# Kernel optimization log

Measured on AMD Instinct MI355X. Metric: run time of the kernel, lower is better.

The kernel has to match this reference:

```python
import jax, jax.numpy as jnp
import numpy as np

NUM_AUTHORS = 100000
NUM_PAPERS = 150000
EMB_DIM = 64
N_EDGES = 3200000
BATCH = 65536
EPS = 1e-8


def setup_inputs() -> dict:
    key = jax.random.key(0)
    k = jax.random.split(key, 6)
    return {
        "author_emb": jax.random.normal(k[0], (NUM_AUTHORS, EMB_DIM), dtype=jnp.float32) * 0.01,
        "paper_emb": jax.random.normal(k[1], (NUM_PAPERS, EMB_DIM), dtype=jnp.float32) * 0.01,
        "authors": jax.random.randint(k[2], (BATCH,), 0, NUM_AUTHORS),
        "papers": jax.random.randint(k[3], (BATCH,), 0, NUM_PAPERS),
        "edge_author": jax.random.randint(k[4], (N_EDGES,), 0, NUM_AUTHORS),
        "edge_paper": jax.random.randint(k[5], (N_EDGES,), 0, NUM_PAPERS),
    }


def _write_conv(a_emb, p_emb, edge_author, edge_paper, norm, u_sw, i_sw):
    """GCN-style bipartite conv with symmetric degree normalization and
    degree-gated self term (u_sw/i_sw ~= 1 only for isolated nodes)."""
    # messages author -> paper over 'like' edges
    msg_ap = a_emb[edge_author] * norm[:, None]            # [E, D]
    new_p = i_sw * p_emb + jax.ops.segment_sum(msg_ap, edge_paper, num_segments=NUM_PAPERS)
    # messages paper -> author over 'rev_like' edges
    msg_pa = p_emb[edge_paper] * norm[:, None]             # [E, D]
    new_a = u_sw * a_emb + jax.ops.segment_sum(msg_pa, edge_author, num_segments=NUM_AUTHORS)
    return new_a, new_p


def reference(author_emb, paper_emb, authors, papers, edge_author, edge_paper):
    ones_e = jnp.ones((N_EDGES,), dtype=jnp.float32)
    author_deg = jax.ops.segment_sum(ones_e, edge_author, num_segments=NUM_AUTHORS)  # out-deg 'like'
    paper_deg = jax.ops.segment_sum(ones_e, edge_paper, num_segments=NUM_PAPERS)     # out-deg 'rev_like'
    u_sw = (1.0 - author_deg / (author_deg + EPS))[:, None]   # [Na, 1]
    i_sw = (1.0 - paper_deg / (paper_deg + EPS))[:, None]     # [Np, 1]
    # symmetric normalization per edge: 1/sqrt(deg_a * deg_p)
    norm = jax.lax.rsqrt((author_deg[edge_author] + EPS) * (paper_deg[edge_paper] + EPS))  # [E]

    a1, p1 = _write_conv(author_emb, paper_emb, edge_author, edge_paper, norm, u_sw, i_sw)
    a2, p2 = _write_conv(a1, p1, edge_author, edge_paper, norm, u_sw, i_sw)

    final_author = author_emb + a1 + a2   # l_author = [0,1,2]
    final_paper = paper_emb + p1 + p2     # l_paper = [0,1,2]

    latest_author = final_author[authors]  # [B, D]
    latest_paper = final_paper[papers]     # [B, D]
    predict = jax.nn.sigmoid(jnp.sum(latest_author * latest_paper, axis=1))  # [B]
    return predict, latest_author, latest_paper
```

## Files before the change

kernel.cpp:

```cpp
#include <hip/hip_runtime.h>
#include <hip/hip_bf16.h>
#include <math.h>

#define NA 100000
#define NP 150000
#define EMB 64
#define NE 3200000
#define BATCH 65536
#define EPS 1e-8f
#define F8 128.0f
#define INVF8 (1.0f / 128.0f)

#define SH_A 8
#define SH_P 9
#define NB_A ((NA + (1 << SH_A) - 1) >> SH_A)
#define NB_P ((NP + (1 << SH_P) - 1) >> SH_P)
#define NBT (NB_A + NB_P)
#define CAP_A 9216
#define CAP_P 12288
#define TOT_A (NB_A * CAP_A)
#define TOT_P (NB_P * CAP_P)
#define PACK_SH 18
#define PACK_MASK ((1u << PACK_SH) - 1)
#define CHUNK 8192
#define NOENT 0xFFFFFFFFu

typedef float f32x2 __attribute__((ext_vector_type(2)));

#if defined(__has_builtin)
#if __has_builtin(__builtin_amdgcn_cvt_pk_f32_fp8) && __has_builtin(__builtin_amdgcn_cvt_pk_fp8_f32)
#define HW_FP8 1
#endif
#endif

__device__ inline unsigned pk_fp8x4(float a, float b, float c, float d) {
#ifdef HW_FP8
    int t = __builtin_amdgcn_cvt_pk_fp8_f32(a, b, 0, false);
    t = __builtin_amdgcn_cvt_pk_fp8_f32(c, d, t, true);
    return (unsigned)t;
#else
    auto enc = [](float x) -> unsigned {
        union { float f; unsigned u; } t; t.f = x;
        unsigned s = t.u >> 31; int e = (int)((t.u >> 23) & 0xFF) - 127;
        unsigned m = (t.u >> 20) & 7;
        int E = e + 7;
        if (E <= 0) return s << 7;
        if (E > 15) { E = 15; m = 7; }
        return (s << 7) | ((unsigned)E << 3) | m;
    };
    return enc(a) | (enc(b) << 8) | (enc(c) << 16) | (enc(d) << 24);
#endif
}

__device__ inline f32x2 up_fp8x2(unsigned v, bool hi) {
#ifdef HW_FP8
    return hi ? __builtin_amdgcn_cvt_pk_f32_fp8((int)v, true)
              : __builtin_amdgcn_cvt_pk_f32_fp8((int)v, false);
#else
    auto dec = [](unsigned b) -> float {
        unsigned s = b >> 7, e = (b >> 3) & 0xF, m = b & 7;
        if (e == 0) return (s ? -1.0f : 1.0f) * (float)m * 0.001953125f;
        union { unsigned u; float f; } t;
        t.u = (s << 31) | ((e + 120) << 23) | (m << 20);
        return t.f;
    };
    unsigned sh = hi ? 16 : 0;
    f32x2 r;
    r.x = dec((v >> sh) & 0xFF);
    r.y = dec((v >> (sh + 8)) & 0xFF);
    return r;
#endif
}

__device__ inline unsigned pack_bf16(float a, float b) {
    __hip_bfloat16 ha = __float2bfloat16(a);
    __hip_bfloat16 hb = __float2bfloat16(b);
    unsigned ua = *(unsigned short*)&ha;
    unsigned ub = *(unsigned short*)&hb;
    return ua | (ub << 16);
}

__device__ inline float bf_lo(unsigned u) { return __uint_as_float(u << 16); }
__device__ inline float bf_hi(unsigned u) { return __uint_as_float(u & 0xffff0000u); }


__global__ void init_cur(int* __restrict__ bcur, uint2* __restrict__ sa0,
                         uint2* __restrict__ sp0, uint2* __restrict__ sa1,
                         uint2* __restrict__ sp1) {
    int i = blockIdx.x * blockDim.x + threadIdx.x;
    if (i < NB_A) bcur[i] = i * CAP_A;
    else if (i < NBT) bcur[i] = (i - NB_A) * CAP_P;
    if (i < 8)       sa0[(size_t)NA * 8 + i]        = uint2{0, 0};
    else if (i < 16) sp0[(size_t)NP * 8 + (i - 8)]  = uint2{0, 0};
    else if (i < 24) sa1[(size_t)NA * 8 + (i - 16)] = uint2{0, 0};
    else if (i < 32) sp1[(size_t)NP * 8 + (i - 24)] = uint2{0, 0};
}


__global__ void __launch_bounds__(512) stage_kernel(
        const int* __restrict__ ea, const int* __restrict__ ep,
        int* __restrict__ bcur,
        unsigned* __restrict__ stg_a, unsigned* __restrict__ stg_p) {
    __shared__ unsigned lsbuf[2 * CHUNK];
    __shared__ int hh[NBT];
    __shared__ int lbase[NBT];
    __shared__ int gbase[NBT];
    __shared__ int tsum[512];
    int t = threadIdx.x;

    for (int i = t; i < NBT; i += 512) hh[i] = 0;
    __syncthreads();
    int e0 = blockIdx.x * CHUNK;
    int e1 = min(e0 + CHUNK, NE);
    for (int e = e0 + t; e < e1; e += 512) {
        atomicAdd(&hh[ea[e] >> SH_A], 1);
        atomicAdd(&hh[NB_A + (ep[e] >> SH_P)], 1);
    }
    __syncthreads();

    int v0 = (2 * t < NBT) ? hh[2 * t] : 0;
    int v1 = (2 * t + 1 < NBT) ? hh[2 * t + 1] : 0;
    tsum[t] = v0 + v1;
    __syncthreads();
    for (int o = 1; o < 512; o <<= 1) {
        int v = (t >= o) ? tsum[t - o] : 0;
        __syncthreads();
        tsum[t] += v;
        __syncthreads();
    }
    int excl = (t == 0) ? 0 : tsum[t - 1];
    if (2 * t < NBT) lbase[2 * t] = excl;
    if (2 * t + 1 < NBT) lbase[2 * t + 1] = excl + v0;
    __syncthreads();

    for (int i = t; i < NBT; i += 512) {
        int c = hh[i];
        gbase[i] = c ? atomicAdd(&bcur[i], c) : 0;
    }
    __syncthreads();
    for (int i = t; i < NBT; i += 512) hh[i] = lbase[i];
    __syncthreads();

    for (int e = e0 + t; e < e1; e += 512) {
        int a = ea[e], p = ep[e];
        int ba = a >> SH_A;
        int bp = NB_A + (p >> SH_P);
        int sa = atomicAdd(&hh[ba], 1);
        lsbuf[sa] = ((unsigned)(a & ((1 << SH_A) - 1)) << PACK_SH) | (unsigned)p;
        int sp = atomicAdd(&hh[bp], 1);
        lsbuf[sp] = ((unsigned)(p & ((1 << SH_P) - 1)) << PACK_SH) | (unsigned)a;
    }
    __syncthreads();

    int wv = t >> 6, ln = t & 63;
    for (int i = wv; i < NBT; i += 8) {
        int lb = lbase[i];
        int c = hh[i] - lb;
        int gb = gbase[i];
        if (i < NB_A) {
            for (int j = ln; j < c; j += 64) stg_a[gb + j] = lsbuf[lb + j];
        } else {
            for (int j = ln; j < c; j += 64) stg_p[gb + j] = lsbuf[lb + j];
        }
    }
}


template <int S, int CAP, int NNODES, int KMAX>
__device__ __forceinline__ void build_side(
    const unsigned* __restrict__ stg, const int* __restrict__ bend, int b,
    int* __restrict__ off, float* __restrict__ rs, int* __restrict__ dg,
    int* __restrict__ csr, const float4* __restrict__ emb, uint2* __restrict__ sfp8,
    int* cnt , int* tsum , int* ls ) {
    int t = threadIdx.x;
    int node0 = b * S;
    int nloc = min(S, NNODES - node0);
    int p0 = b * CAP, p1 = bend[b];
    int nent = p1 - p0;

    unsigned ent[KMAX];
    #pragma unroll
    for (int k = 0; k < KMAX; ++k) {
        int i = t + k * 512;
        ent[k] = (i < nent) ? stg[p0 + i] : NOENT;
    }

    for (int i = t; i < S; i += 512) cnt[i] = 0;
    __syncthreads();
    #pragma unroll
    for (int k = 0; k < KMAX; ++k)
        if (ent[k] != NOENT) atomicAdd(&cnt[ent[k] >> PACK_SH], 1);
    __syncthreads();

    int val = (t < S) ? cnt[t] : 0;
    tsum[t] = val;
    __syncthreads();
    for (int o = 1; o < 512; o <<= 1) {
        int v = (t >= o) ? tsum[t - o] : 0;
        __syncthreads();
        tsum[t] += v;
        __syncthreads();
    }
    int excl = (t == 0) ? 0 : tsum[t - 1];
    if (t < S) {
        if (t < nloc) {
            off[node0 + t] = p0 + excl;
            dg[node0 + t] = val;
            rs[node0 + t] = rsqrtf((float)val + EPS);
        }
        cnt[t] = excl;
    }
    __syncthreads();

    #pragma unroll
    for (int k = 0; k < KMAX; ++k)
        if (ent[k] != NOENT) {
            int slot = atomicAdd(&cnt[ent[k] >> PACK_SH], 1);
            ls[slot] = (int)((ent[k] & PACK_MASK) << 6);
        }
    __syncthreads();

    int rounded = (nent + 3) & ~3;
    for (int i = t * 4; i < rounded; i += 2048) {
        int4 w = {ls[i], ls[i + 1], ls[i + 2], ls[i + 3]};
        *(int4*)(csr + p0 + i) = w;
    }

    int q = t & 7;
    for (int ln = t >> 3; ln < nloc; ln += 64) {
        int n = node0 + ln;
        float r = rs[n] * F8;
        float4 v0 = emb[n * 16 + q * 2];
        float4 v1 = emb[n * 16 + q * 2 + 1];
        uint2 o;
        o.x = pk_fp8x4(r * v0.x, r * v0.y, r * v0.z, r * v0.w);
        o.y = pk_fp8x4(r * v1.x, r * v1.y, r * v1.z, r * v1.w);
        sfp8[(size_t)n * 8 + q] = o;
    }
}

__global__ void __launch_bounds__(512) build_all(
                          const unsigned* __restrict__ stg_a,
                          const unsigned* __restrict__ stg_p,
                          const int* __restrict__ bcur,
                          int* __restrict__ off_a, float* __restrict__ rs_a,
                          int* __restrict__ dg_a, int* __restrict__ csr_a,
                          int* __restrict__ off_p, float* __restrict__ rs_p,
                          int* __restrict__ dg_p, int* __restrict__ csr_p,
                          const float4* __restrict__ a_emb, const float4* __restrict__ p_emb,
                          uint2* __restrict__ sa0, uint2* __restrict__ sp0) {
    __shared__ int ls[CAP_P];
    __shared__ int cnt[512];
    __shared__ int tsum[512];
    int b = blockIdx.x;
    if (b < NB_A)
        build_side<256, CAP_A, NA, (CAP_A + 511) / 512>(
            stg_a, bcur, b, off_a, rs_a, dg_a, csr_a, a_emb, sa0, cnt, tsum, ls);
    else
        build_side<512, CAP_P, NP, (CAP_P + 511) / 512>(
            stg_p, bcur + NB_A, b - NB_A, off_p, rs_p, dg_p, csr_p, p_emb, sp0, cnt, tsum, ls);
}

template <int LAYER, bool IS_PAPER>
__global__ void pullg(const int* __restrict__ off_s, const int* __restrict__ dg_s,
                      const int* __restrict__ csr_s, const float* __restrict__ rs_s,
                      const uint2* __restrict__ src,
                      const float4* __restrict__ emb,
                      uint4* __restrict__ io,
                      uint2* __restrict__ sout) {
    constexpr int NW = (IS_PAPER ? NP : NA) / 8;
    int wid = (int)(((size_t)blockIdx.x * blockDim.x + threadIdx.x) >> 6);
    if (wid >= NW) return;
    int lane = threadIdx.x & 63;
    int g = lane >> 3;
    int q = lane & 7;
    int n = wid * 8 + g;

    const char* srcb = (const char*)src;
    unsigned zoff = (unsigned)(IS_PAPER ? NA : NP) << 6;

    int start = off_s[n];
    int deg = dg_s[n];
    float rsd = rs_s[n];
    unsigned q8 = (unsigned)(q << 3);

    f32x2 acc[4];
    acc[0] = f32x2{0, 0}; acc[1] = f32x2{0, 0};
    acc[2] = f32x2{0, 0}; acc[3] = f32x2{0, 0};

    unsigned myid_next = (q < deg) ? (unsigned)csr_s[start + q] : zoff;
    for (int t = 0; t < deg; t += 8) {
        unsigned myid = myid_next;
        {
            unsigned idv = (unsigned)csr_s[start + t + 8 + q];
            myid_next = (t + 8 + q < deg) ? idv : zoff;
        }
        uint2 v[8];
        #pragma unroll
        for (int k = 0; k < 8; ++k) {
            unsigned ide = (unsigned)__shfl((int)myid, k, 8);
            v[k] = *(const uint2*)(srcb + (ide | q8));
        }
        #pragma unroll
        for (int k = 0; k < 8; ++k) {
            acc[0] += up_fp8x2(v[k].x, false);
            acc[1] += up_fp8x2(v[k].x, true);
            acc[2] += up_fp8x2(v[k].y, false);
            acc[3] += up_fp8x2(v[k].y, true);
        }
    }

    float inv = rsd * INVF8;
    if (LAYER == 1) {
        int f4 = n * 16 + q * 2;
        float4 e0 = emb[f4];
        float4 e1 = emb[f4 + 1];
        float d = (float)deg;
        float sw = 1.0f - d / (d + EPS);
        float l1[8];
        l1[0] = sw * e0.x + inv * acc[0].x;
        l1[1] = sw * e0.y + inv * acc[0].y;
        l1[2] = sw * e0.z + inv * acc[1].x;
        l1[3] = sw * e0.w + inv * acc[1].y;
        l1[4] = sw * e1.x + inv * acc[2].x;
        l1[5] = sw * e1.y + inv * acc[2].y;
        l1[6] = sw * e1.z + inv * acc[3].x;
        l1[7] = sw * e1.w + inv * acc[3].y;
        float gs = F8 * rsd;
        uint2 sv;
        sv.x = pk_fp8x4(gs * l1[0], gs * l1[1], gs * l1[2], gs * l1[3]);
        sv.y = pk_fp8x4(gs * l1[4], gs * l1[5], gs * l1[6], gs * l1[7]);
        sout[(size_t)n * 8 + q] = sv;
        float c = 1.0f + sw;
        uint4 ov;
        ov.x = pack_bf16(e0.x + c * l1[0], e0.y + c * l1[1]);
        ov.y = pack_bf16(e0.z + c * l1[2], e0.w + c * l1[3]);
        ov.z = pack_bf16(e1.x + c * l1[4], e1.y + c * l1[5]);
        ov.w = pack_bf16(e1.z + c * l1[6], e1.w + c * l1[7]);
        io[(size_t)n * 8 + q] = ov;
    } else {
        uint4 pr = io[(size_t)n * 8 + q];
        uint4 ov;
        ov.x = pack_bf16(bf_lo(pr.x) + inv * acc[0].x, bf_hi(pr.x) + inv * acc[0].y);
        ov.y = pack_bf16(bf_lo(pr.y) + inv * acc[1].x, bf_hi(pr.y) + inv * acc[1].y);
        ov.z = pack_bf16(bf_lo(pr.z) + inv * acc[2].x, bf_hi(pr.z) + inv * acc[2].y);
        ov.w = pack_bf16(bf_lo(pr.w) + inv * acc[3].x, bf_hi(pr.w) + inv * acc[3].y);
        io[(size_t)n * 8 + q] = ov;
    }
}


__global__ void gather_kernel(const unsigned short* __restrict__ fa,
                              const unsigned short* __restrict__ fp,
                              const int* __restrict__ authors, const int* __restrict__ papers,
                              float* __restrict__ out, int batch) {
    int t = blockIdx.x * blockDim.x + threadIdx.x;
    int b = t >> 6;
    int d = t & 63;
    if (b >= batch) return;
    float la = __uint_as_float((unsigned)fa[authors[b] * EMB + d] << 16);
    float lp = __uint_as_float((unsigned)fp[papers[b] * EMB + d] << 16);
    out[batch + b * EMB + d] = la;
    out[batch + batch * EMB + b * EMB + d] = lp;
    float prod = la * lp;
    #pragma unroll
    for (int off = 32; off > 0; off >>= 1)
        prod += __shfl_down(prod, off, 64);
    if (d == 0)
        out[b] = 1.0f / (1.0f + expf(-prod));
}


extern "C" void kernel_launch(void* const* d_in, const int* in_sizes, int n_in,
                              void* d_out, int out_size, void* d_ws, size_t ws_size,
                              hipStream_t stream) {
    const float* author_emb = (const float*)d_in[0];
    const float* paper_emb  = (const float*)d_in[1];
    const int*   authors    = (const int*)d_in[2];
    const int*   papers     = (const int*)d_in[3];
    const int*   edge_a     = (const int*)d_in[4];
    const int*   edge_p     = (const int*)d_in[5];
    float* out = (float*)d_out;

    char* ws = (char*)d_ws;
    size_t woff = 0;
    auto alloc = [&](size_t bytes) {
        void* p = ws + woff;
        woff += (bytes + 255) & ~(size_t)255;
        return p;
    };
    int*   bcur    = (int*)alloc(NBT * sizeof(int));
    int*   off_a   = (int*)alloc(NA * sizeof(int));
    int*   off_p   = (int*)alloc(NP * sizeof(int));
    int*   dg_a    = (int*)alloc(NA * sizeof(int));
    int*   dg_p    = (int*)alloc(NP * sizeof(int));
    float* rs_a    = (float*)alloc(NA * sizeof(float));
    float* rs_p    = (float*)alloc(NP * sizeof(float));
    int*   csr_a   = (int*)alloc((size_t)TOT_A * sizeof(int));
    int*   csr_p   = (int*)alloc((size_t)TOT_P * sizeof(int));
    uint2* sa0     = (uint2*)alloc((size_t)(NA + 1) * EMB);
    uint2* sp0     = (uint2*)alloc((size_t)(NP + 1) * EMB);
    uint2* sa1     = (uint2*)alloc((size_t)(NA + 1) * EMB);
    uint2* sp1     = (uint2*)alloc((size_t)(NP + 1) * EMB);
    uint4* a1      = (uint4*)alloc((size_t)NA * EMB * 2);
    uint4* p1      = (uint4*)alloc((size_t)NP * EMB * 2);
    unsigned* stg_a = (unsigned*)alloc((size_t)TOT_A * sizeof(unsigned));
    unsigned* stg_p = (unsigned*)alloc((size_t)TOT_P * sizeof(unsigned));
    (void)ws_size;

    init_cur<<<(NBT + 255) / 256, 256, 0, stream>>>(bcur, sa0, sp0, sa1, sp1);
    stage_kernel<<<(NE + CHUNK - 1) / CHUNK, 512, 0, stream>>>(edge_a, edge_p, bcur, stg_a, stg_p);
    build_all<<<NBT, 512, 0, stream>>>(stg_a, stg_p, bcur,
                                       off_a, rs_a, dg_a, csr_a,
                                       off_p, rs_p, dg_p, csr_p,
                                       (const float4*)author_emb, (const float4*)paper_emb,
                                       sa0, sp0);

    const unsigned GP = (unsigned)(((long long)(NP / 8) * 64 + 255) / 256);
    const unsigned GA = (unsigned)(((long long)(NA / 8) * 64 + 255) / 256);

    pullg<1, true><<<GP, 256, 0, stream>>>(
        off_p, dg_p, csr_p, rs_p, sa0, (const float4*)paper_emb, p1, sp1);
    pullg<1, false><<<GA, 256, 0, stream>>>(
        off_a, dg_a, csr_a, rs_a, sp0, (const float4*)author_emb, a1, sa1);

    pullg<2, true><<<GP, 256, 0, stream>>>(
        off_p, dg_p, csr_p, rs_p, sa1, (const float4*)paper_emb, p1, nullptr);
    pullg<2, false><<<GA, 256, 0, stream>>>(
        off_a, dg_a, csr_a, rs_a, sp1, (const float4*)author_emb, a1, nullptr);

    {
        long long total = (long long)BATCH * 64;
        gather_kernel<<<(unsigned)((total + 255) / 256), 256, 0, stream>>>(
            (const unsigned short*)a1, (const unsigned short*)p1, authors, papers, out, BATCH);
    }
}
```

Before: 267.8 us.

## Halve staging chunk, cache edges in registers, flatten scatter with binary search

```diff
diff --git a/kernel.cpp b/kernel.cpp
--- a/kernel.cpp
+++ b/kernel.cpp
@@ -22,7 +22,8 @@
 #define TOT_P (NB_P * CAP_P)
 #define PACK_SH 18
 #define PACK_MASK ((1u << PACK_SH) - 1)
-#define CHUNK 8192
+#define CHUNK 4096
+#define EPT 8
 #define NOENT 0xFFFFFFFFu
 
 typedef float f32x2 __attribute__((ext_vector_type(2)));
@@ -103,18 +104,30 @@
         unsigned* __restrict__ stg_a, unsigned* __restrict__ stg_p) {
     __shared__ unsigned lsbuf[2 * CHUNK];
     __shared__ int hh[NBT];
-    __shared__ int lbase[NBT];
+    __shared__ int lbase[NBT + 1];
     __shared__ int gbase[NBT];
     __shared__ int tsum[512];
     int t = threadIdx.x;
 
-    for (int i = t; i < NBT; i += 512) hh[i] = 0;
-    __syncthreads();
     int e0 = blockIdx.x * CHUNK;
     int e1 = min(e0 + CHUNK, NE);
-    for (int e = e0 + t; e < e1; e += 512) {
-        atomicAdd(&hh[ea[e] >> SH_A], 1);
-        atomicAdd(&hh[NB_A + (ep[e] >> SH_P)], 1);
+    int av[EPT], pv[EPT];
+    #pragma unroll
+    for (int k = 0; k < EPT; ++k) {
+        int e = e0 + t + k * 512;
+        bool ok = (e < e1);
+        av[k] = ok ? ea[e] : -1;
+        pv[k] = ok ? ep[e] : -1;
+    }
+
+    for (int i = t; i < NBT; i += 512) hh[i] = 0;
+    __syncthreads();
+    #pragma unroll
+    for (int k = 0; k < EPT; ++k) {
+        if (av[k] >= 0) {
+            atomicAdd(&hh[av[k] >> SH_A], 1);
+            atomicAdd(&hh[NB_A + (pv[k] >> SH_P)], 1);
+        }
     }
     __syncthreads();
 
@@ -131,6 +144,7 @@
     int excl = (t == 0) ? 0 : tsum[t - 1];
     if (2 * t < NBT) lbase[2 * t] = excl;
     if (2 * t + 1 < NBT) lbase[2 * t + 1] = excl + v0;
+    if (t == 511) lbase[NBT] = tsum[511];
     __syncthreads();
 
     for (int i = t; i < NBT; i += 512) {
@@ -141,27 +155,30 @@
     for (int i = t; i < NBT; i += 512) hh[i] = lbase[i];
     __syncthreads();
 
-    for (int e = e0 + t; e < e1; e += 512) {
-        int a = ea[e], p = ep[e];
-        int ba = a >> SH_A;
-        int bp = NB_A + (p >> SH_P);
-        int sa = atomicAdd(&hh[ba], 1);
-        lsbuf[sa] = ((unsigned)(a & ((1 << SH_A) - 1)) << PACK_SH) | (unsigned)p;
-        int sp = atomicAdd(&hh[bp], 1);
-        lsbuf[sp] = ((unsigned)(p & ((1 << SH_P) - 1)) << PACK_SH) | (unsigned)a;
-    }
-    __syncthreads();
-
-    int wv = t >> 6, ln = t & 63;
-    for (int i = wv; i < NBT; i += 8) {
-        int lb = lbase[i];
-        int c = hh[i] - lb;
-        int gb = gbase[i];
-        if (i < NB_A) {
-            for (int j = ln; j < c; j += 64) stg_a[gb + j] = lsbuf[lb + j];
-        } else {
-            for (int j = ln; j < c; j += 64) stg_p[gb + j] = lsbuf[lb + j];
-        }
+    #pragma unroll
+    for (int k = 0; k < EPT; ++k) {
+        if (av[k] >= 0) {
+            int ba = av[k] >> SH_A;
+            int bp = NB_A + (pv[k] >> SH_P);
+            int sa = atomicAdd(&hh[ba], 1);
+            lsbuf[sa] = ((unsigned)(av[k] & ((1 << SH_A) - 1)) << PACK_SH) | (unsigned)pv[k];
+            int sp = atomicAdd(&hh[bp], 1);
+            lsbuf[sp] = ((unsigned)(pv[k] & ((1 << SH_P) - 1)) << PACK_SH) | (unsigned)av[k];
+        }
+    }
+    __syncthreads();
+
+    int total = lbase[NBT];
+    for (int i = t; i < total; i += 512) {
+        int lo = 0, hi = NBT;
+        while (hi - lo > 1) {
+            int mid = (lo + hi) >> 1;
+            if (lbase[mid] <= i) lo = mid; else hi = mid;
+        }
+        int pos = gbase[lo] + (i - lbase[lo]);
+        unsigned v = lsbuf[i];
+        if (lo < NB_A) stg_a[pos] = v;
+        else           stg_p[pos] = v;
     }
 }
 
```

Result: slower. 279.2 us (+4.2%).
